# Kernel optimization log

Measured on AMD Instinct MI355X. Metric: run time of the kernel, lower is better.

## Reference

```python
import jax, jax.numpy as jnp
import numpy as np

B, C, H, W = 64, 256, 28, 28
EPS = 1e-8  # torch CosineSimilarity eps


def _make_grids(key):
    # coordinate meshgrid [2, H, W]: channel 0 = y, channel 1 = x
    yy, xx = jnp.meshgrid(jnp.arange(H, dtype=jnp.float32),
                          jnp.arange(W, dtype=jnp.float32), indexing='ij')
    coords = jnp.stack([yy, xx])  # [2, H, W]
    k1, k2 = jax.random.split(key)
    scale = jax.random.uniform(k1, (B, 1, 1, 1), minval=0.9, maxval=1.1)
    shift = jax.random.uniform(k2, (B, 2, 1, 1), minval=0.0, maxval=5.0)
    return coords[None] * scale + shift  # [B, 2, H, W]


def setup_inputs() -> dict:
    key = jax.random.key(0)
    ks = jax.random.split(key, 6)
    return {
        'y1': jax.random.normal(ks[0], (B, C, H, W), jnp.float32),
        'y2': jax.random.normal(ks[1], (B, C, H, W), jnp.float32),
        'z1': jax.random.normal(ks[2], (B, C, H, W), jnp.float32),
        'z2': jax.random.normal(ks[3], (B, C, H, W), jnp.float32),
        'view1_grid': _make_grids(ks[4]),
        'view2_grid': _make_grids(ks[5]),
    }


def _grid_distances(grid1, grid2):
    # grid*: [B, 2, H, W] -> [B, 2, N]; pairwise euclidean dist [B, N, N]
    g1 = grid1.reshape(grid1.shape[0], 2, -1)
    g2 = grid2.reshape(grid2.shape[0], 2, -1)
    dy = g1[:, 0, :, None] - g2[:, 0, None, :]
    dx = g1[:, 1, :, None] - g2[:, 1, None, :]
    return jnp.sqrt(dy * dy + dx * dx)


def _cosine_sim_pairwise(a, b):
    # a, b: [B, C, N]; cosine sim over channel dim -> [B, N, N]
    num = jnp.einsum('bcn,bcm->bnm', a, b)
    na = jnp.linalg.norm(a, axis=1)  # [B, N]
    nb = jnp.linalg.norm(b, axis=1)  # [B, N]
    den = jnp.maximum(na[:, :, None] * nb[:, None, :], EPS)
    return num / den


def _masked_mean(sim, mask):
    m = mask.astype(sim.dtype)
    return jnp.sum(sim * m) / jnp.sum(m)


def reference(y1, y2, z1, z2, view1_grid, view2_grid):
    distance_thr = 0.7
    y1f = y1.reshape(y1.shape[0], y1.shape[1], -1)
    y2f = y2.reshape(y2.shape[0], y2.shape[1], -1)
    z1f = z1.reshape(z1.shape[0], z1.shape[1], -1)
    z2f = z2.reshape(z2.shape[0], z2.shape[1], -1)

    distances = _grid_distances(view1_grid, view2_grid)  # [B, N, N]
    view1_bin = jnp.linalg.norm(view1_grid[..., 1, 1] - view1_grid[..., 0, 0], axis=-1)  # [B]
    view2_bin = jnp.linalg.norm(view2_grid[..., 1, 1] - view2_grid[..., 0, 0], axis=-1)  # [B]

    view1_mask = (distances / view1_bin[:, None, None]) <= distance_thr
    view2_mask = (distances / view2_bin[:, None, None]) <= distance_thr

    view1_loss = _masked_mean(_cosine_sim_pairwise(y1f, z2f), view1_mask)
    view2_loss = _masked_mean(_cosine_sim_pairwise(y2f, z1f), view2_mask)
    return -1.0 * (view1_loss + view2_loss)
```

## Files before the change

### kernel.cpp

```cpp
#include <hip/hip_runtime.h>
#include <hip/hip_bf16.h>

#define BB   64
#define CC   256
#define NPIX 784
#define BNP  (BB * NPIX)
#define SLOTS 128

__global__ __launch_bounds__(256) void zt_k(
    const float* __restrict__ z1, const float* __restrict__ z2,
    float* __restrict__ zt, float* __restrict__ zn2) {
    __shared__ float lds[32 * 257];
    __shared__ float part[8][32];

    int bx = blockIdx.x;
    int nt = bx % 25;
    int t  = bx / 25;
    int b  = t & 63;
    int arr = t >> 6;
    int nlim = (nt == 24) ? 16 : 32;

    const float* in = (arr ? z2 : z1) + (size_t)b * CC * NPIX + nt * 32;
    int tid  = threadIdx.x;
    int n4   = tid & 7;
    int subc = tid >> 3;
    int nn   = 4 * n4;

#pragma unroll
    for (int k = 0; k < 8; k++) {
        int c = subc + 32 * k;
        float4 v = {0.f, 0.f, 0.f, 0.f};
        if (nn < nlim) v = *(const float4*)(in + (size_t)c * NPIX + nn);
        lds[(nn + 0) * 257 + c] = v.x;
        lds[(nn + 1) * 257 + c] = v.y;
        lds[(nn + 2) * 257 + c] = v.z;
        lds[(nn + 3) * 257 + c] = v.w;
    }
    __syncthreads();

    {
        int nl = tid & 31, cq = tid >> 5;
        float s = 0.f;
#pragma unroll 8
        for (int sc = 0; sc < 32; sc++) {
            float v = lds[nl * 257 + cq * 32 + sc];
            s = fmaf(v, v, s);
        }
        part[cq][nl] = s;
    }

    float* outb = zt + ((size_t)arr * BB + b) * ((size_t)NPIX * CC)
                     + (size_t)nt * 32 * CC;
    int lane = tid & 63, wv = tid >> 6;
    int c4 = lane & 15, nq = (lane >> 4) & 3;
#pragma unroll
    for (int cq2 = 0; cq2 < 4; cq2++) {
#pragma unroll
        for (int nb = 0; nb < 2; nb++) {
            int n = 8 * wv + 4 * nb + nq;
            if (n < nlim) {
                int cc0 = 64 * cq2 + 4 * c4;
                float4 v;
                v.x = lds[n * 257 + cc0 + 0];
                v.y = lds[n * 257 + cc0 + 1];
                v.z = lds[n * 257 + cc0 + 2];
                v.w = lds[n * 257 + cc0 + 3];
                *(float4*)(outb + (size_t)n * CC + cc0) = v;
            }
        }
    }
    __syncthreads();
    if (tid < nlim) {
        float s = part[0][tid] + part[1][tid] + part[2][tid] + part[3][tid]
                + part[4][tid] + part[5][tid] + part[6][tid] + part[7][tid];
        zn2[(size_t)arr * BNP + (size_t)b * NPIX + nt * 32 + tid] = s;
    }
}

__global__ __launch_bounds__(1024, 8) void pairs_k(
    const float* __restrict__ y1, const float* __restrict__ y2,
    const float* __restrict__ zt, const float* __restrict__ zn2,
    const float* __restrict__ g1g, const float* __restrict__ g2g,
    double* __restrict__ acc) {
    __shared__ float  ylds[16 * 256];
    __shared__ double shs[16];
    __shared__ int    shc[16];

    int tid  = threadIdx.x;
    int lane = tid & 63, wv = tid >> 6;
    int bx   = blockIdx.x;
    int loss = (bx >= 3136) ? 1 : 0;
    int rem  = bx - loss * 3136;
    int b    = rem / 49;
    int ig   = rem - b * 49;
    int i0   = 16 * ig;

    const float* Yg = (loss ? y2 : y1) + (size_t)b * CC * NPIX;
    if (tid < 256) {
        const float* row = Yg + (size_t)tid * NPIX + i0;
#pragma unroll
        for (int q = 0; q < 4; q++) {
            float4 v = *(const float4*)(row + 4 * q);
            ylds[(4 * q + 0) * 256 + tid] = v.x;
            ylds[(4 * q + 1) * 256 + tid] = v.y;
            ylds[(4 * q + 2) * 256 + tid] = v.z;
            ylds[(4 * q + 3) * 256 + tid] = v.w;
        }
    }

    const float* g1 = g1g + (size_t)b * 2 * NPIX;
    const float* g2 = g2g + (size_t)b * 2 * NPIX;
    int i = i0 + wv;
    float g1y = g1[i];
    float g1x = g1[NPIX + i];

    const float* gb = loss ? g2 : g1;
    float d0  = gb[29] - gb[0];
    float d1  = gb[NPIX + 29] - gb[NPIX];
    float bin = __fsqrt_rn(__fadd_rn(__fmul_rn(d0, d0), __fmul_rn(d1, d1)));

    float t2y = g2[0], t2x = g2[NPIX];
    float s2y = g2[28] - g2[0];
    float s2x = g2[NPIX + 1] - g2[NPIX];
    float r  = 0.7f * bin * 1.0002f + 1e-4f;
    float cy = (g1y - t2y) / s2y;
    float cx = (g1x - t2x) / s2x;
    float ry = r / s2y + 0.05f;
    float rx = r / s2x + 0.05f;
    int jy0 = max(0,  (int)ceilf(cy - ry));
    int jy1 = min(27, (int)floorf(cy + ry));
    int jx0 = max(0,  (int)ceilf(cx - rx));
    int jx1 = min(27, (int)floorf(cx + rx));
    int dyr = jy1 - jy0, dxr = jx1 - jx0;

    int dyl = lane >> 2, dxl = lane & 3;
    bool pass = false;
    if (lane < 16 && dyl <= dyr && dxl <= dxr) {
        int jc = (jy0 + dyl) * 28 + jx0 + dxl;
        float dy = g1y - g2[jc];
        float dx = g1x - g2[NPIX + jc];
        float d  = __fsqrt_rn(__fadd_rn(__fmul_rn(dy, dy), __fmul_rn(dx, dx)));
        pass = (__fdiv_rn(d, bin) <= 0.7f);
    }
    unsigned long long m = __ballot(pass);
    int cnt = __builtin_popcountll(m);

    __syncthreads();

    int gl = lane & 15, g = lane >> 4;
    const float4* Yr = (const float4*)(ylds + wv * 256);
    float4 ya = Yr[gl], yb = Yr[gl + 16], yc = Yr[gl + 32], yd = Yr[gl + 48];

    float p = ya.x * ya.x;
    p = fmaf(ya.y, ya.y, p); p = fmaf(ya.z, ya.z, p); p = fmaf(ya.w, ya.w, p);
    p = fmaf(yb.x, yb.x, p); p = fmaf(yb.y, yb.y, p); p = fmaf(yb.z, yb.z, p);
    p = fmaf(yb.w, yb.w, p);
    p = fmaf(yc.x, yc.x, p); p = fmaf(yc.y, yc.y, p); p = fmaf(yc.z, yc.z, p);
    p = fmaf(yc.w, yc.w, p);
    p = fmaf(yd.x, yd.x, p); p = fmaf(yd.y, yd.y, p); p = fmaf(yd.z, yd.z, p);
    p = fmaf(yd.w, yd.w, p);
#pragma unroll
    for (int off = 1; off < 16; off <<= 1) p += __shfl_xor(p, off);
    float na = __fsqrt_rn(p);

    const float* Zb = zt  + ((size_t)(1 - loss) * BB + b) * ((size_t)NPIX * CC);
    const float* zn = zn2 + ((size_t)(1 - loss) * BB + b) * NPIX;

    double ssum = 0.0;
#pragma unroll
    for (int rr = 0; rr < 4; rr++) {
        int mr = (int)((m >> (4 * rr)) & 15ull);
        if (!mr) continue;
        int s   = 4 * rr + g;
        bool val = (mr >> g) & 1;
        int j = val ? ((jy0 + (s >> 2)) * 28 + jx0 + (s & 3)) : 0;
        const float4* Z4 = (const float4*)(Zb + (size_t)j * CC);
        float4 za = Z4[gl], zb_ = Z4[gl + 16], zc = Z4[gl + 32], zd = Z4[gl + 48];
        float nb2 = zn[j];
        float dp = ya.x * za.x;
        dp = fmaf(ya.y, za.y, dp); dp = fmaf(ya.z, za.z, dp);
        dp = fmaf(ya.w, za.w, dp);
        dp = fmaf(yb.x, zb_.x, dp); dp = fmaf(yb.y, zb_.y, dp);
        dp = fmaf(yb.z, zb_.z, dp); dp = fmaf(yb.w, zb_.w, dp);
        dp = fmaf(yc.x, zc.x, dp); dp = fmaf(yc.y, zc.y, dp);
        dp = fmaf(yc.z, zc.z, dp); dp = fmaf(yc.w, zc.w, dp);
        dp = fmaf(yd.x, zd.x, dp); dp = fmaf(yd.y, zd.y, dp);
        dp = fmaf(yd.z, zd.z, dp); dp = fmaf(yd.w, zd.w, dp);
#pragma unroll
        for (int off = 1; off < 16; off <<= 1) dp += __shfl_xor(dp, off);
        float den = fmaxf(na * __fsqrt_rn(nb2), 1e-8f);
        float sim = __fdividef(dp, den);
        if (val) ssum += (double)sim;
    }
    ssum += __shfl_xor(ssum, 16);
    ssum += __shfl_xor(ssum, 32);

    if (lane == 0) { shs[wv] = ssum; shc[wv] = cnt; }
    __syncthreads();
    if (tid == 0) {
        double s = 0.0; int c = 0;
#pragma unroll
        for (int k = 0; k < 16; k++) { s += shs[k]; c += shc[k]; }
        double* slot = acc + (size_t)(bx & (SLOTS - 1)) * 4;
        atomicAdd(&slot[loss * 2],     s);
        atomicAdd(&slot[loss * 2 + 1], (double)c);
    }
}

__global__ void fin_k(const double* __restrict__ acc, float* __restrict__ out) {
    int lane = threadIdx.x;
    double s0 = 0, m0 = 0, s1 = 0, m1 = 0;
    for (int s = lane; s < SLOTS; s += 64) {
        const double* p = acc + (size_t)s * 4;
        s0 += p[0]; m0 += p[1]; s1 += p[2]; m1 += p[3];
    }
#pragma unroll
    for (int off = 32; off; off >>= 1) {
        s0 += __shfl_xor(s0, off); m0 += __shfl_xor(m0, off);
        s1 += __shfl_xor(s1, off); m1 += __shfl_xor(m1, off);
    }
    if (lane == 0) out[0] = (float)(-(s0 / m0 + s1 / m1));
}

extern "C" void kernel_launch(void* const* d_in, const int* in_sizes, int n_in,
                              void* d_out, int out_size, void* d_ws, size_t ws_size,
                              hipStream_t stream) {
    const float* y1 = (const float*)d_in[0];
    const float* y2 = (const float*)d_in[1];
    const float* z1 = (const float*)d_in[2];
    const float* z2 = (const float*)d_in[3];
    const float* g1 = (const float*)d_in[4];
    const float* g2 = (const float*)d_in[5];
    float* out = (float*)d_out;

    char* ws = (char*)d_ws;
    double* acc = (double*)ws;
    float*  zn2 = (float*)(ws + 4096);
    float*  zt  = (float*)(ws + 4096 + 2 * BNP * sizeof(float));

    hipMemsetAsync(acc, 0, SLOTS * 4 * sizeof(double), stream);

    zt_k<<<3200, 256, 0, stream>>>(z1, z2, zt, zn2);

    pairs_k<<<6272, 1024, 0, stream>>>(y1, y2, zt, zn2, g1, g2, acc);

    fin_k<<<1, 64, 0, stream>>>(acc, out);
}
```

Before: 277.9 us.

## Drop z transpose kernel; gather z columns directly and compute norms inline

Removes the separate transpose kernel that wrote z in [N, C] layout plus its squared norms, so z is no longer read and rewritten in full before the main kernel. The pairs kernel now gathers each neighbour's channel vector straight from the original [C, N] layout with strided scalar loads and accumulates the z norm alongside the dot product. This trades a full extra pass over z for uncoalesced strided gathers, with each lane loading 16 scalars spaced NPIX apart. Invalid lanes now point at a real neighbour index instead of index 0.

```diff
diff --git a/kernel.cpp b/kernel.cpp
--- a/kernel.cpp
+++ b/kernel.cpp
@@ -7,79 +7,9 @@
 #define BNP  (BB * NPIX)
 #define SLOTS 128
 
-__global__ __launch_bounds__(256) void zt_k(
-    const float* __restrict__ z1, const float* __restrict__ z2,
-    float* __restrict__ zt, float* __restrict__ zn2) {
-    __shared__ float lds[32 * 257];
-    __shared__ float part[8][32];
-
-    int bx = blockIdx.x;
-    int nt = bx % 25;
-    int t  = bx / 25;
-    int b  = t & 63;
-    int arr = t >> 6;
-    int nlim = (nt == 24) ? 16 : 32;
-
-    const float* in = (arr ? z2 : z1) + (size_t)b * CC * NPIX + nt * 32;
-    int tid  = threadIdx.x;
-    int n4   = tid & 7;
-    int subc = tid >> 3;
-    int nn   = 4 * n4;
-
-#pragma unroll
-    for (int k = 0; k < 8; k++) {
-        int c = subc + 32 * k;
-        float4 v = {0.f, 0.f, 0.f, 0.f};
-        if (nn < nlim) v = *(const float4*)(in + (size_t)c * NPIX + nn);
-        lds[(nn + 0) * 257 + c] = v.x;
-        lds[(nn + 1) * 257 + c] = v.y;
-        lds[(nn + 2) * 257 + c] = v.z;
-        lds[(nn + 3) * 257 + c] = v.w;
-    }
-    __syncthreads();
-
-    {
-        int nl = tid & 31, cq = tid >> 5;
-        float s = 0.f;
-#pragma unroll 8
-        for (int sc = 0; sc < 32; sc++) {
-            float v = lds[nl * 257 + cq * 32 + sc];
-            s = fmaf(v, v, s);
-        }
-        part[cq][nl] = s;
-    }
-
-    float* outb = zt + ((size_t)arr * BB + b) * ((size_t)NPIX * CC)
-                     + (size_t)nt * 32 * CC;
-    int lane = tid & 63, wv = tid >> 6;
-    int c4 = lane & 15, nq = (lane >> 4) & 3;
-#pragma unroll
-    for (int cq2 = 0; cq2 < 4; cq2++) {
-#pragma unroll
-        for (int nb = 0; nb < 2; nb++) {
-            int n = 8 * wv + 4 * nb + nq;
-            if (n < nlim) {
-                int cc0 = 64 * cq2 + 4 * c4;
-                float4 v;
-                v.x = lds[n * 257 + cc0 + 0];
-                v.y = lds[n * 257 + cc0 + 1];
-                v.z = lds[n * 257 + cc0 + 2];
-                v.w = lds[n * 257 + cc0 + 3];
-                *(float4*)(outb + (size_t)n * CC + cc0) = v;
-            }
-        }
-    }
-    __syncthreads();
-    if (tid < nlim) {
-        float s = part[0][tid] + part[1][tid] + part[2][tid] + part[3][tid]
-                + part[4][tid] + part[5][tid] + part[6][tid] + part[7][tid];
-        zn2[(size_t)arr * BNP + (size_t)b * NPIX + nt * 32 + tid] = s;
-    }
-}
-
 __global__ __launch_bounds__(1024, 8) void pairs_k(
     const float* __restrict__ y1, const float* __restrict__ y2,
-    const float* __restrict__ zt, const float* __restrict__ zn2,
+    const float* __restrict__ z1, const float* __restrict__ z2,
     const float* __restrict__ g1g, const float* __restrict__ g2g,
     double* __restrict__ acc) {
     __shared__ float  ylds[16 * 256];
@@ -163,8 +93,7 @@
     for (int off = 1; off < 16; off <<= 1) p += __shfl_xor(p, off);
     float na = __fsqrt_rn(p);
 
-    const float* Zb = zt  + ((size_t)(1 - loss) * BB + b) * ((size_t)NPIX * CC);
-    const float* zn = zn2 + ((size_t)(1 - loss) * BB + b) * NPIX;
+    const float* Zg = (loss ? z1 : z2) + (size_t)b * CC * NPIX;
 
     double ssum = 0.0;
 #pragma unroll
@@ -173,22 +102,51 @@
         if (!mr) continue;
         int s   = 4 * rr + g;
         bool val = (mr >> g) & 1;
-        int j = val ? ((jy0 + (s >> 2)) * 28 + jx0 + (s & 3)) : 0;
-        const float4* Z4 = (const float4*)(Zb + (size_t)j * CC);
-        float4 za = Z4[gl], zb_ = Z4[gl + 16], zc = Z4[gl + 32], zd = Z4[gl + 48];
-        float nb2 = zn[j];
+        int j = val ? ((jy0 + (s >> 2)) * 28 + jx0 + (s & 3))
+                    : (jy0 * 28 + jx0);
+        const float* Zc = Zg + j;
+        int cb = 4 * gl;
+        float4 za, zb_, zc, zd;
+        za.x  = Zc[(size_t)(cb + 0) * NPIX];
+        za.y  = Zc[(size_t)(cb + 1) * NPIX];
+        za.z  = Zc[(size_t)(cb + 2) * NPIX];
+        za.w  = Zc[(size_t)(cb + 3) * NPIX];
+        zb_.x = Zc[(size_t)(cb + 64) * NPIX];
+        zb_.y = Zc[(size_t)(cb + 65) * NPIX];
+        zb_.z = Zc[(size_t)(cb + 66) * NPIX];
+        zb_.w = Zc[(size_t)(cb + 67) * NPIX];
+        zc.x  = Zc[(size_t)(cb + 128) * NPIX];
+        zc.y  = Zc[(size_t)(cb + 129) * NPIX];
+        zc.z  = Zc[(size_t)(cb + 130) * NPIX];
+        zc.w  = Zc[(size_t)(cb + 131) * NPIX];
+        zd.x  = Zc[(size_t)(cb + 192) * NPIX];
+        zd.y  = Zc[(size_t)(cb + 193) * NPIX];
+        zd.z  = Zc[(size_t)(cb + 194) * NPIX];
+        zd.w  = Zc[(size_t)(cb + 195) * NPIX];
+
         float dp = ya.x * za.x;
-        dp = fmaf(ya.y, za.y, dp); dp = fmaf(ya.z, za.z, dp);
-        dp = fmaf(ya.w, za.w, dp);
-        dp = fmaf(yb.x, zb_.x, dp); dp = fmaf(yb.y, zb_.y, dp);
-        dp = fmaf(yb.z, zb_.z, dp); dp = fmaf(yb.w, zb_.w, dp);
-        dp = fmaf(yc.x, zc.x, dp); dp = fmaf(yc.y, zc.y, dp);
-        dp = fmaf(yc.z, zc.z, dp); dp = fmaf(yc.w, zc.w, dp);
-        dp = fmaf(yd.x, zd.x, dp); dp = fmaf(yd.y, zd.y, dp);
-        dp = fmaf(yd.z, zd.z, dp); dp = fmaf(yd.w, zd.w, dp);
-#pragma unroll
-        for (int off = 1; off < 16; off <<= 1) dp += __shfl_xor(dp, off);
-        float den = fmaxf(na * __fsqrt_rn(nb2), 1e-8f);
+        float zz = za.x * za.x;
+        dp = fmaf(ya.y, za.y, dp);  zz = fmaf(za.y, za.y, zz);
+        dp = fmaf(ya.z, za.z, dp);  zz = fmaf(za.z, za.z, zz);
+        dp = fmaf(ya.w, za.w, dp);  zz = fmaf(za.w, za.w, zz);
+        dp = fmaf(yb.x, zb_.x, dp); zz = fmaf(zb_.x, zb_.x, zz);
+        dp = fmaf(yb.y, zb_.y, dp); zz = fmaf(zb_.y, zb_.y, zz);
+        dp = fmaf(yb.z, zb_.z, dp); zz = fmaf(zb_.z, zb_.z, zz);
+        dp = fmaf(yb.w, zb_.w, dp); zz = fmaf(zb_.w, zb_.w, zz);
+        dp = fmaf(yc.x, zc.x, dp);  zz = fmaf(zc.x, zc.x, zz);
+        dp = fmaf(yc.y, zc.y, dp);  zz = fmaf(zc.y, zc.y, zz);
+        dp = fmaf(yc.z, zc.z, dp);  zz = fmaf(zc.z, zc.z, zz);
+        dp = fmaf(yc.w, zc.w, dp);  zz = fmaf(zc.w, zc.w, zz);
+        dp = fmaf(yd.x, zd.x, dp);  zz = fmaf(zd.x, zd.x, zz);
+        dp = fmaf(yd.y, zd.y, dp);  zz = fmaf(zd.y, zd.y, zz);
+        dp = fmaf(yd.z, zd.z, dp);  zz = fmaf(zd.z, zd.z, zz);
+        dp = fmaf(yd.w, zd.w, dp);  zz = fmaf(zd.w, zd.w, zz);
+#pragma unroll
+        for (int off = 1; off < 16; off <<= 1) {
+            dp += __shfl_xor(dp, off);
+            zz += __shfl_xor(zz, off);
+        }
+        float den = fmaxf(na * __fsqrt_rn(zz), 1e-8f);
         float sim = __fdividef(dp, den);
         if (val) ssum += (double)sim;
     }
@@ -233,16 +191,10 @@
     const float* g2 = (const float*)d_in[5];
     float* out = (float*)d_out;
 
-    char* ws = (char*)d_ws;
-    double* acc = (double*)ws;
-    float*  zn2 = (float*)(ws + 4096);
-    float*  zt  = (float*)(ws + 4096 + 2 * BNP * sizeof(float));
-
+    double* acc = (double*)d_ws;
     hipMemsetAsync(acc, 0, SLOTS * 4 * sizeof(double), stream);
 
-    zt_k<<<3200, 256, 0, stream>>>(z1, z2, zt, zn2);
-
-    pairs_k<<<6272, 1024, 0, stream>>>(y1, y2, zt, zn2, g1, g2, acc);
+    pairs_k<<<6272, 1024, 0, stream>>>(y1, y2, z1, z2, g1, g2, acc);
 
     fin_k<<<1, 64, 0, stream>>>(acc, out);
 }
```

Result: slower. 495.0 us (+78.1%).
